# Kernel optimization log

Hardware: AMD Instinct MI355X
Metric: run time of the kernel (lower is better)

## Reference

```python
import jax, jax.numpy as jnp
from jax import lax
import numpy as np

NUM_POINT = 1024
RADIUS = 0.4
NSAMPLE = 32


def setup_inputs() -> dict:
    key = jax.random.key(0)
    ks = jax.random.split(key, 16)
    B, N, C = 8, 16384, 64
    chans = [67, 64, 128, 256]
    inp = {
        "points_xyz": jax.random.normal(ks[0], (B, N, 3), jnp.float32),
        "features": jax.random.normal(ks[1], (B, C, N), jnp.float32),
    }
    ki = 2
    for l, (cin, cout) in enumerate(zip(chans[:-1], chans[1:])):
        inp[f"W{l}"] = jax.random.normal(ks[ki], (cout, cin), jnp.float32) * (1.0 / np.sqrt(cin)); ki += 1
        inp[f"b{l}"] = jax.random.normal(ks[ki], (cout,), jnp.float32) * 0.02; ki += 1
        inp[f"s{l}"] = jax.random.uniform(ks[ki], (cout,), jnp.float32, 0.5, 1.5); ki += 1
        inp[f"t{l}"] = jax.random.normal(ks[ki], (cout,), jnp.float32) * 0.02; ki += 1
    return inp


def farthest_point_sample(xyz, npoint):
    # xyz: (B, N, 3) -> idx (B, npoint) int32. D-FPS starting at index 0.
    B, N, _ = xyz.shape

    def step(carry, _):
        dists, farthest = carry  # (B,N), (B,)
        centroid = jnp.take_along_axis(xyz, farthest[:, None, None], axis=1)  # (B,1,3)
        d = jnp.sum((xyz - centroid) ** 2, axis=-1)  # (B,N)
        dists = jnp.minimum(dists, d)
        nxt = jnp.argmax(dists, axis=-1).astype(jnp.int32)
        return (dists, nxt), farthest

    init = (jnp.full((B, N), 1e10, xyz.dtype), jnp.zeros((B,), jnp.int32))
    _, idx = lax.scan(step, init, None, length=npoint)
    return idx.T  # (B, npoint)


def ball_query(points_xyz, new_xyz, radius, nsample):
    # First-nsample-in-index-order points within radius; pad with first found
    # (semantics of the CUDA ball_query kernel in PointNet++/mmdet3d).
    B, N, _ = points_xyz.shape
    d2 = jnp.sum((new_xyz[:, :, None, :] - points_xyz[:, None, :, :]) ** 2, axis=-1)  # (B,M,N)
    arange = jnp.arange(N, dtype=jnp.float32)
    key = jnp.where(d2 <= radius * radius, arange, jnp.float32(N))
    neg_k, _ = lax.top_k(-key, nsample)  # smallest nsample keys
    idx = (-neg_k).astype(jnp.int32)  # (B,M,K)
    first = idx[..., :1]
    idx = jnp.where(idx < N, idx, first)  # pad empty slots with first neighbor
    return jnp.clip(idx, 0, N - 1)


def query_and_group(points_xyz, new_xyz, features, idx, use_xyz=True):
    # points_xyz (B,N,3), new_xyz (B,M,3), features (B,C,N), idx (B,M,K)
    B, N, _ = points_xyz.shape
    M, K = idx.shape[1], idx.shape[2]
    flat = idx.reshape(B, M * K)
    gxyz = jnp.take_along_axis(points_xyz, flat[:, :, None], axis=1).reshape(B, M, K, 3)
    gxyz = gxyz - new_xyz[:, :, None, :]  # relative coords
    gxyz = jnp.transpose(gxyz, (0, 3, 1, 2))  # (B,3,M,K)
    gfeat = jnp.take_along_axis(features, flat[:, None, :], axis=2).reshape(B, -1, M, K)
    if use_xyz:
        return jnp.concatenate([gxyz, gfeat], axis=1)  # (B, 3+C, M, K)
    return gfeat


def mlp_layer(x, W, b, s, t):
    # 1x1 Conv2d + folded BatchNorm (per-channel scale/shift) + ReLU
    y = jnp.einsum("oc,bcmk->bomk", W, x) + b[None, :, None, None]
    y = y * s[None, :, None, None] + t[None, :, None, None]
    return jax.nn.relu(y)


def reference(points_xyz, features, W0, b0, s0, t0, W1, b1, s1, t1, W2, b2, s2, t2):
    indices = farthest_point_sample(points_xyz, NUM_POINT)  # (B,M)
    new_xyz = jnp.take_along_axis(points_xyz, indices[:, :, None], axis=1)  # (B,M,3)
    idx = ball_query(points_xyz, new_xyz, RADIUS, NSAMPLE)  # (B,M,K)
    g = query_and_group(points_xyz, new_xyz, features, idx, use_xyz=True)  # (B,67,M,K)
    h = mlp_layer(g, W0, b0, s0, t0)
    h = mlp_layer(h, W1, b1, s1, t1)
    h = mlp_layer(h, W2, b2, s2, t2)  # (B,256,M,K)
    new_features = jnp.max(h, axis=-1)  # max pool over K -> (B,256,M)
    return new_xyz, new_features, indices
```

## Files before the change

### kernel.cpp

```cpp
#include <hip/hip_runtime.h>
#include <stdint.h>

#define NB 8
#define NPT 16384
#define NM 1024
#define NK 32

#define WS_W0T 0
#define WS_B0  (WS_W0T + 4288)
#define WS_W1T (WS_B0 + 64)
#define WS_B1  (WS_W1T + 8192)
#define WS_W2T (WS_B1 + 128)
#define WS_B2  (WS_W2T + 32768)
#define WS_IDX (WS_B2 + 256)
#define WS_NXYZ (WS_IDX + 8192)
#define WS_BALL (WS_NXYZ + 24576)

#define OUT_XYZ 0
#define OUT_FEAT 24576
#define OUT_IDX (24576 + 2097152)

__global__ void prep_weights(const float* __restrict__ W0, const float* __restrict__ b0,
                             const float* __restrict__ s0, const float* __restrict__ t0,
                             const float* __restrict__ W1, const float* __restrict__ b1,
                             const float* __restrict__ s1, const float* __restrict__ t1,
                             const float* __restrict__ W2, const float* __restrict__ b2,
                             const float* __restrict__ s2, const float* __restrict__ t2,
                             float* __restrict__ ws) {
    int id = blockIdx.x * 256 + threadIdx.x;
    if (id < 4288) { int c = id >> 6, o = id & 63;  ws[WS_W0T + id] = W0[o * 67 + c] * s0[o]; return; }
    id -= 4288;
    if (id < 64)   { ws[WS_B0 + id] = fmaf(b0[id], s0[id], t0[id]); return; }
    id -= 64;
    if (id < 8192) { int c = id >> 7, o = id & 127; ws[WS_W1T + id] = W1[o * 64 + c] * s1[o]; return; }
    id -= 8192;
    if (id < 128)  { ws[WS_B1 + id] = fmaf(b1[id], s1[id], t1[id]); return; }
    id -= 128;
    if (id < 32768){ int c = id >> 8, o = id & 255; ws[WS_W2T + id] = W2[o * 128 + c] * s2[o]; return; }
    id -= 32768;
    if (id < 256)  { ws[WS_B2 + id] = fmaf(b2[id], s2[id], t2[id]); return; }
}

#define FOREACH16(M) M(0) M(1) M(2) M(3) M(4) M(5) M(6) M(7) \
                     M(8) M(9) M(10) M(11) M(12) M(13) M(14) M(15)

template <int CTRL>
__device__ __forceinline__ uint32_t dpp_max_step(uint32_t v) {
    uint32_t o = (uint32_t)__builtin_amdgcn_update_dpp((int)v, (int)v, CTRL, 0xf, 0xf, false);
    return v > o ? v : o;
}
__device__ __forceinline__ uint32_t wave_max_u32(uint32_t v) {
    v = dpp_max_step<0x111>(v);
    v = dpp_max_step<0x112>(v);
    v = dpp_max_step<0x114>(v);
    v = dpp_max_step<0x118>(v);
    v = dpp_max_step<0x142>(v);
    v = dpp_max_step<0x143>(v);
    return v;
}
__device__ __forceinline__ uint32_t row_max_u32(uint32_t v) {
    v = dpp_max_step<0x111>(v);
    v = dpp_max_step<0x112>(v);
    v = dpp_max_step<0x114>(v);
    v = dpp_max_step<0x118>(v);
    return v;
}

__global__ __attribute__((amdgpu_flat_work_group_size(1024, 1024)))
void fps10_kernel(const float* __restrict__ xyz, int* __restrict__ out_idx) {
    __shared__ float2 pxy[NPT];
    __shared__ uint2 s_red[2][16];
    int b = blockIdx.x, t = threadIdx.x;
    const float* __restrict__ Xp = xyz + (size_t)b * NPT * 3;

#define DECL_PT(j) float pz##j, dd##j;
    FOREACH16(DECL_PT)
#undef DECL_PT

#define LOAD_PT(j) { int p = t + (j) * 1024; \
        float x = Xp[p * 3 + 0], y = Xp[p * 3 + 1]; \
        pz##j = Xp[p * 3 + 2]; \
        pxy[p] = make_float2(x, y); \
        dd##j = 1e10f; }
    FOREACH16(LOAD_PT)
#undef LOAD_PT
    __syncthreads();

    int farthest = 0;
    float cx = Xp[0], cy = Xp[1], cz = Xp[2];
    int lane = t & 63, w = t >> 6;
    for (int it = 0; it < NM; ++it) {
        if (t == 0) out_idx[b * NM + it] = farthest;
        float best = -1.0f; int bi = 0;
#define STEP_PT(j) { \
        float2 q = pxy[t + (j) * 1024]; \
        float dx = __fsub_rn(q.x, cx); \
        float dy = __fsub_rn(q.y, cy); \
        float dz = __fsub_rn(pz##j, cz); \
        float d  = __fadd_rn(__fadd_rn(__fmul_rn(dx, dx), __fmul_rn(dy, dy)), __fmul_rn(dz, dz)); \
        dd##j = fminf(dd##j, d); \
        if (dd##j > best) { best = dd##j; bi = t + (j) * 1024; } }
        FOREACH16(STEP_PT)
#undef STEP_PT
        uint32_t bbits = __float_as_uint(best);
        uint32_t wmax = __builtin_amdgcn_readlane(wave_max_u32(bbits), 63);
        uint32_t cand = (bbits == wmax) ? ~(uint32_t)bi : 0u;
        uint32_t cwin = __builtin_amdgcn_readlane(wave_max_u32(cand), 63);
        if (lane == 0) s_red[it & 1][w] = make_uint2(cwin, wmax);
        __syncthreads();
        uint2 e = s_red[it & 1][lane & 15];
        uint32_t hmax = __builtin_amdgcn_readlane(row_max_u32(e.y), 15);
        uint32_t c2 = (e.y == hmax) ? e.x : 0u;
        uint32_t c2w = __builtin_amdgcn_readlane(row_max_u32(c2), 15);
        int widx = (int)(~c2w);
        farthest = widx;
        float2 cc = pxy[widx];
        cx = cc.x; cy = cc.y;
        cz = Xp[(size_t)widx * 3 + 2];
    }
}

__global__ void gather_newxyz(const float* __restrict__ xyz, const int* __restrict__ idx_ws,
                              float* __restrict__ nxyz_ws, float* __restrict__ out_xyz,
                              float* __restrict__ out_idx_f) {
    int id = blockIdx.x * 256 + threadIdx.x;
    if (id >= NB * NM) return;
    int b = id / NM;
    int p = idx_ws[id];
    const float* Xp = xyz + ((size_t)b * NPT + p) * 3;
    float x = Xp[0], y = Xp[1], z = Xp[2];
    nxyz_ws[id * 3 + 0] = x; nxyz_ws[id * 3 + 1] = y; nxyz_ws[id * 3 + 2] = z;
    out_xyz[id * 3 + 0] = x; out_xyz[id * 3 + 1] = y; out_xyz[id * 3 + 2] = z;
    out_idx_f[id] = (float)p;
}

__global__ __launch_bounds__(256) void ball_query_kernel(const float* __restrict__ xyz,
                                                         const float* __restrict__ nxyz,
                                                         int* __restrict__ ball) {
    int blk = blockIdx.x;
    int b = blk >> 10;
    int t = threadIdx.x;
    const float* Xp = xyz + (size_t)b * NPT * 3;
    float cx = nxyz[blk * 3 + 0], cy = nxyz[blk * 3 + 1], cz = nxyz[blk * 3 + 2];
    const float r2 = (float)(0.4 * 0.4);
    uint64_t mask = 0;
    int base = t * 64;
    const float4* q = (const float4*)(Xp + (size_t)base * 3);
#pragma unroll 4
    for (int c = 0; c < 16; c++) {
        float4 A = q[c * 3 + 0], B = q[c * 3 + 1], C = q[c * 3 + 2];
        float xs[4] = {A.x, A.w, B.z, C.y};
        float ys[4] = {A.y, B.x, B.w, C.z};
        float zs[4] = {A.z, B.y, C.x, C.w};
#pragma unroll
        for (int u = 0; u < 4; u++) {
            float dx = __fsub_rn(xs[u], cx);
            float dy = __fsub_rn(ys[u], cy);
            float dz = __fsub_rn(zs[u], cz);
            float d2 = __fadd_rn(__fadd_rn(__fmul_rn(dx, dx), __fmul_rn(dy, dy)), __fmul_rn(dz, dz));
            if (d2 <= r2) mask |= (1ull << (c * 4 + u));
        }
    }
    int cnt = __popcll(mask);
    int scan = cnt;
    for (int off = 1; off < 64; off <<= 1) {
        int nv = __shfl_up(scan, off);
        if ((t & 63) >= off) scan += nv;
    }
    __shared__ int s_wsum[4];
    __shared__ int s_hit[32];
    int w = t >> 6;
    if ((t & 63) == 63) s_wsum[w] = scan;
    __syncthreads();
    int woff = 0;
    for (int i = 0; i < 4; i++) if (i < w) woff += s_wsum[i];
    int excl = woff + scan - cnt;
    uint64_t mm = mask; int pos = excl;
    while (mm && pos < 32) {
        int j = __ffsll((long long)mm) - 1;
        s_hit[pos] = base + j;
        pos++;
        mm &= mm - 1;
    }
    __syncthreads();
    int total = s_wsum[0] + s_wsum[1] + s_wsum[2] + s_wsum[3];
    if (t < 32) {
        int first = s_hit[0];
        ball[blk * NK + t] = (t < total) ? s_hit[t] : first;
    }
}

__global__ __attribute__((amdgpu_flat_work_group_size(256, 256), amdgpu_waves_per_eu(3, 3)))
void fused_mlp_kernel(const float* __restrict__ xyz,
                      const float* __restrict__ feats,
                      const float* __restrict__ ws_f,
                      const int* __restrict__ ball,
                      const float* __restrict__ nxyz,
                      float* __restrict__ out_feat) {
    int blk = blockIdx.x;
    int b = blk >> 9;
    int m0 = (blk & 511) * 2;
    int t = threadIdx.x;
    int k = t & 31, g = t >> 5;
    __shared__ float u[2][128][32];
    __shared__ float h1[2][64][32];
    __shared__ int sidx[2][32];
    const float* W0t = ws_f + WS_W0T; const float* b0f = ws_f + WS_B0;
    const float* W1t = ws_f + WS_W1T; const float* b1f = ws_f + WS_B1;
    const float* W2t = ws_f + WS_W2T; const float* b2f = ws_f + WS_B2;

    if (t < 64) {
        int ctr = t >> 5;
        sidx[ctr][t & 31] = ball[((size_t)b * NM + m0 + ctr) * NK + (t & 31)];
    }
    __syncthreads();

    const float* Xp = xyz + (size_t)b * NPT * 3;
    if (g < 6) {
        int ctr = g / 3, dim = g % 3;
        float cc = nxyz[((size_t)b * NM + m0 + ctr) * 3 + dim];
        u[ctr][dim][k] = Xp[sidx[ctr][k] * 3 + dim] - cc;
    }
    const float* Fp = feats + (size_t)b * 64 * NPT;
#pragma unroll
    for (int i = 0; i < 8; i++) {
        int c = g + 8 * i;
        u[0][3 + c][k] = Fp[(size_t)c * NPT + sidx[0][k]];
        u[1][3 + c][k] = Fp[(size_t)c * NPT + sidx[1][k]];
    }
    __syncthreads();

    {
        float acc0[8], acc1[8];
#pragma unroll
        for (int i = 0; i < 8; i++) { acc0[i] = b0f[g * 8 + i]; acc1[i] = acc0[i]; }
#pragma unroll 4
        for (int c = 0; c < 67; c++) {
            float xv0 = u[0][c][k], xv1 = u[1][c][k];
            const float* wr = W0t + c * 64 + g * 8;
            float4 wa = *(const float4*)(wr), wb = *(const float4*)(wr + 4);
            acc0[0] = fmaf(wa.x, xv0, acc0[0]); acc1[0] = fmaf(wa.x, xv1, acc1[0]);
            acc0[1] = fmaf(wa.y, xv0, acc0[1]); acc1[1] = fmaf(wa.y, xv1, acc1[1]);
            acc0[2] = fmaf(wa.z, xv0, acc0[2]); acc1[2] = fmaf(wa.z, xv1, acc1[2]);
            acc0[3] = fmaf(wa.w, xv0, acc0[3]); acc1[3] = fmaf(wa.w, xv1, acc1[3]);
            acc0[4] = fmaf(wb.x, xv0, acc0[4]); acc1[4] = fmaf(wb.x, xv1, acc1[4]);
            acc0[5] = fmaf(wb.y, xv0, acc0[5]); acc1[5] = fmaf(wb.y, xv1, acc1[5]);
            acc0[6] = fmaf(wb.z, xv0, acc0[6]); acc1[6] = fmaf(wb.z, xv1, acc1[6]);
            acc0[7] = fmaf(wb.w, xv0, acc0[7]); acc1[7] = fmaf(wb.w, xv1, acc1[7]);
        }
#pragma unroll
        for (int i = 0; i < 8; i++) {
            h1[0][g * 8 + i][k] = fmaxf(acc0[i], 0.0f);
            h1[1][g * 8 + i][k] = fmaxf(acc1[i], 0.0f);
        }
    }
    __syncthreads();

    {
        float acc0[16], acc1[16];
#pragma unroll
        for (int i = 0; i < 16; i++) { acc0[i] = b1f[g * 16 + i]; acc1[i] = acc0[i]; }
#pragma unroll 4
        for (int c = 0; c < 64; c++) {
            float xv0 = h1[0][c][k], xv1 = h1[1][c][k];
            const float4* wr = (const float4*)(W1t + c * 128 + g * 16);
#pragma unroll
            for (int q = 0; q < 4; q++) {
                float4 wv = wr[q];
                acc0[q * 4 + 0] = fmaf(wv.x, xv0, acc0[q * 4 + 0]); acc1[q * 4 + 0] = fmaf(wv.x, xv1, acc1[q * 4 + 0]);
                acc0[q * 4 + 1] = fmaf(wv.y, xv0, acc0[q * 4 + 1]); acc1[q * 4 + 1] = fmaf(wv.y, xv1, acc1[q * 4 + 1]);
                acc0[q * 4 + 2] = fmaf(wv.z, xv0, acc0[q * 4 + 2]); acc1[q * 4 + 2] = fmaf(wv.z, xv1, acc1[q * 4 + 2]);
                acc0[q * 4 + 3] = fmaf(wv.w, xv0, acc0[q * 4 + 3]); acc1[q * 4 + 3] = fmaf(wv.w, xv1, acc1[q * 4 + 3]);
            }
        }
        __syncthreads();
#pragma unroll
        for (int i = 0; i < 16; i++) {
            u[0][g * 16 + i][k] = fmaxf(acc0[i], 0.0f);
            u[1][g * 16 + i][k] = fmaxf(acc1[i], 0.0f);
        }
    }
    __syncthreads();

#pragma unroll
    for (int half = 0; half < 2; half++) {
        float acc0[16], acc1[16];
#pragma unroll
        for (int i = 0; i < 16; i++) { acc0[i] = b2f[g * 32 + half * 16 + i]; acc1[i] = acc0[i]; }
#pragma unroll 4
        for (int c = 0; c < 128; c++) {
            float xv0 = u[0][c][k], xv1 = u[1][c][k];
            const float4* wr = (const float4*)(W2t + c * 256 + g * 32 + half * 16);
#pragma unroll
            for (int q = 0; q < 4; q++) {
                float4 wv = wr[q];
                acc0[q * 4 + 0] = fmaf(wv.x, xv0, acc0[q * 4 + 0]); acc1[q * 4 + 0] = fmaf(wv.x, xv1, acc1[q * 4 + 0]);
                acc0[q * 4 + 1] = fmaf(wv.y, xv0, acc0[q * 4 + 1]); acc1[q * 4 + 1] = fmaf(wv.y, xv1, acc1[q * 4 + 1]);
                acc0[q * 4 + 2] = fmaf(wv.z, xv0, acc0[q * 4 + 2]); acc1[q * 4 + 2] = fmaf(wv.z, xv1, acc1[q * 4 + 2]);
                acc0[q * 4 + 3] = fmaf(wv.w, xv0, acc0[q * 4 + 3]); acc1[q * 4 + 3] = fmaf(wv.w, xv1, acc1[q * 4 + 3]);
            }
        }
#pragma unroll
        for (int i = 0; i < 16; i++) {
            float v0 = fmaxf(acc0[i], 0.0f);
            float v1 = fmaxf(acc1[i], 0.0f);
#pragma unroll
            for (int off = 16; off >= 1; off >>= 1) {
                v0 = fmaxf(v0, __shfl_xor(v0, off));
                v1 = fmaxf(v1, __shfl_xor(v1, off));
            }
            if (k == 0) {
                size_t o = (size_t)b * 256 + g * 32 + half * 16 + i;
                out_feat[o * NM + m0]     = v0;
                out_feat[o * NM + m0 + 1] = v1;
            }
        }
    }
}

extern "C" void kernel_launch(void* const* d_in, const int* in_sizes, int n_in,
                              void* d_out, int out_size, void* d_ws, size_t ws_size,
                              hipStream_t stream) {
    const float* xyz   = (const float*)d_in[0];
    const float* feats = (const float*)d_in[1];
    const float* W0 = (const float*)d_in[2];  const float* b0 = (const float*)d_in[3];
    const float* s0 = (const float*)d_in[4];  const float* t0 = (const float*)d_in[5];
    const float* W1 = (const float*)d_in[6];  const float* b1 = (const float*)d_in[7];
    const float* s1 = (const float*)d_in[8];  const float* t1 = (const float*)d_in[9];
    const float* W2 = (const float*)d_in[10]; const float* b2 = (const float*)d_in[11];
    const float* s2 = (const float*)d_in[12]; const float* t2 = (const float*)d_in[13];

    float* ws_f = (float*)d_ws;
    int*   idx_ws  = (int*)(ws_f + WS_IDX);
    float* nxyz_ws = ws_f + WS_NXYZ;
    int*   ball_ws = (int*)(ws_f + WS_BALL);

    float* out_f = (float*)d_out;
    float* out_xyz  = out_f + OUT_XYZ;
    float* out_feat = out_f + OUT_FEAT;
    float* out_idxf = out_f + OUT_IDX;

    prep_weights<<<179, 256, 0, stream>>>(W0, b0, s0, t0, W1, b1, s1, t1, W2, b2, s2, t2, ws_f);
    fps10_kernel<<<NB, 1024, 0, stream>>>(xyz, idx_ws);
    gather_newxyz<<<32, 256, 0, stream>>>(xyz, idx_ws, nxyz_ws, out_xyz, out_idxf);
    ball_query_kernel<<<NB * NM, 256, 0, stream>>>(xyz, nxyz_ws, ball_ws);
    fused_mlp_kernel<<<NB * NM / 2, 256, 0, stream>>>(xyz, feats, ws_f, ball_ws, nxyz_ws, out_feat);
}
```

Before: 2.690 ms.

## Make MLP weight indices wave-uniform so weights load as scalar operands

Each 64-lane wavefront in the fused MLP kernel now covers both centers (32 samples each) and a group of 16 output channels chosen by wave index. readfirstlane makes the weight offset wave-uniform, so the compiler can fetch weights with scalar loads and broadcast them instead of issuing per-lane vector loads. This also drops the doubled per-center accumulators, which lowers register pressure. The cost is more passes over the input activations per thread in layers 2 and 3.

```diff
diff --git a/kernel.cpp b/kernel.cpp
--- a/kernel.cpp
+++ b/kernel.cpp
@@ -202,6 +202,8 @@
     int m0 = (blk & 511) * 2;
     int t = threadIdx.x;
     int k = t & 31, g = t >> 5;
+    int lane = t & 63, wv = t >> 6;
+    int ctr = lane >> 5, k2 = lane & 31;
     __shared__ float u[2][128][32];
     __shared__ float h1[2][64][32];
     __shared__ int sidx[2][32];
@@ -210,16 +212,16 @@
     const float* W2t = ws_f + WS_W2T; const float* b2f = ws_f + WS_B2;
 
     if (t < 64) {
-        int ctr = t >> 5;
-        sidx[ctr][t & 31] = ball[((size_t)b * NM + m0 + ctr) * NK + (t & 31)];
+        int c2 = t >> 5;
+        sidx[c2][t & 31] = ball[((size_t)b * NM + m0 + c2) * NK + (t & 31)];
     }
     __syncthreads();
 
     const float* Xp = xyz + (size_t)b * NPT * 3;
     if (g < 6) {
-        int ctr = g / 3, dim = g % 3;
-        float cc = nxyz[((size_t)b * NM + m0 + ctr) * 3 + dim];
-        u[ctr][dim][k] = Xp[sidx[ctr][k] * 3 + dim] - cc;
+        int c2 = g / 3, dim = g % 3;
+        float cc = nxyz[((size_t)b * NM + m0 + c2) * 3 + dim];
+        u[c2][dim][k] = Xp[sidx[c2][k] * 3 + dim] - cc;
     }
     const float* Fp = feats + (size_t)b * 64 * NPT;
 #pragma unroll
@@ -231,88 +233,61 @@
     __syncthreads();
 
     {
-        float acc0[8], acc1[8];
-#pragma unroll
-        for (int i = 0; i < 8; i++) { acc0[i] = b0f[g * 8 + i]; acc1[i] = acc0[i]; }
+        int ob = __builtin_amdgcn_readfirstlane(wv * 16);
+        float acc[16];
+#pragma unroll
+        for (int i = 0; i < 16; i++) acc[i] = b0f[ob + i];
 #pragma unroll 4
         for (int c = 0; c < 67; c++) {
-            float xv0 = u[0][c][k], xv1 = u[1][c][k];
-            const float* wr = W0t + c * 64 + g * 8;
-            float4 wa = *(const float4*)(wr), wb = *(const float4*)(wr + 4);
-            acc0[0] = fmaf(wa.x, xv0, acc0[0]); acc1[0] = fmaf(wa.x, xv1, acc1[0]);
-            acc0[1] = fmaf(wa.y, xv0, acc0[1]); acc1[1] = fmaf(wa.y, xv1, acc1[1]);
-            acc0[2] = fmaf(wa.z, xv0, acc0[2]); acc1[2] = fmaf(wa.z, xv1, acc1[2]);
-            acc0[3] = fmaf(wa.w, xv0, acc0[3]); acc1[3] = fmaf(wa.w, xv1, acc1[3]);
-            acc0[4] = fmaf(wb.x, xv0, acc0[4]); acc1[4] = fmaf(wb.x, xv1, acc1[4]);
-            acc0[5] = fmaf(wb.y, xv0, acc0[5]); acc1[5] = fmaf(wb.y, xv1, acc1[5]);
-            acc0[6] = fmaf(wb.z, xv0, acc0[6]); acc1[6] = fmaf(wb.z, xv1, acc1[6]);
-            acc0[7] = fmaf(wb.w, xv0, acc0[7]); acc1[7] = fmaf(wb.w, xv1, acc1[7]);
-        }
-#pragma unroll
-        for (int i = 0; i < 8; i++) {
-            h1[0][g * 8 + i][k] = fmaxf(acc0[i], 0.0f);
-            h1[1][g * 8 + i][k] = fmaxf(acc1[i], 0.0f);
-        }
-    }
-    __syncthreads();
-
-    {
-        float acc0[16], acc1[16];
-#pragma unroll
-        for (int i = 0; i < 16; i++) { acc0[i] = b1f[g * 16 + i]; acc1[i] = acc0[i]; }
+            float xv = u[ctr][c][k2];
+            const float* wr = W0t + c * 64 + ob;
+#pragma unroll
+            for (int i = 0; i < 16; i++) acc[i] = fmaf(wr[i], xv, acc[i]);
+        }
+#pragma unroll
+        for (int i = 0; i < 16; i++) h1[ctr][ob + i][k2] = fmaxf(acc[i], 0.0f);
+    }
+    __syncthreads();
+
+#pragma unroll
+    for (int p = 0; p < 2; p++) {
+        int ob = __builtin_amdgcn_readfirstlane(wv * 16 + p * 64);
+        float acc[16];
+#pragma unroll
+        for (int i = 0; i < 16; i++) acc[i] = b1f[ob + i];
 #pragma unroll 4
         for (int c = 0; c < 64; c++) {
-            float xv0 = h1[0][c][k], xv1 = h1[1][c][k];
-            const float4* wr = (const float4*)(W1t + c * 128 + g * 16);
-#pragma unroll
-            for (int q = 0; q < 4; q++) {
-                float4 wv = wr[q];
-                acc0[q * 4 + 0] = fmaf(wv.x, xv0, acc0[q * 4 + 0]); acc1[q * 4 + 0] = fmaf(wv.x, xv1, acc1[q * 4 + 0]);
-                acc0[q * 4 + 1] = fmaf(wv.y, xv0, acc0[q * 4 + 1]); acc1[q * 4 + 1] = fmaf(wv.y, xv1, acc1[q * 4 + 1]);
-                acc0[q * 4 + 2] = fmaf(wv.z, xv0, acc0[q * 4 + 2]); acc1[q * 4 + 2] = fmaf(wv.z, xv1, acc1[q * 4 + 2]);
-                acc0[q * 4 + 3] = fmaf(wv.w, xv0, acc0[q * 4 + 3]); acc1[q * 4 + 3] = fmaf(wv.w, xv1, acc1[q * 4 + 3]);
-            }
-        }
-        __syncthreads();
-#pragma unroll
-        for (int i = 0; i < 16; i++) {
-            u[0][g * 16 + i][k] = fmaxf(acc0[i], 0.0f);
-            u[1][g * 16 + i][k] = fmaxf(acc1[i], 0.0f);
-        }
-    }
-    __syncthreads();
-
-#pragma unroll
-    for (int half = 0; half < 2; half++) {
-        float acc0[16], acc1[16];
-#pragma unroll
-        for (int i = 0; i < 16; i++) { acc0[i] = b2f[g * 32 + half * 16 + i]; acc1[i] = acc0[i]; }
+            float xv = h1[ctr][c][k2];
+            const float* wr = W1t + c * 128 + ob;
+#pragma unroll
+            for (int i = 0; i < 16; i++) acc[i] = fmaf(wr[i], xv, acc[i]);
+        }
+#pragma unroll
+        for (int i = 0; i < 16; i++) u[ctr][ob + i][k2] = fmaxf(acc[i], 0.0f);
+    }
+    __syncthreads();
+
+#pragma unroll
+    for (int p = 0; p < 4; p++) {
+        int ob = __builtin_amdgcn_readfirstlane(wv * 16 + p * 64);
+        float acc[16];
+#pragma unroll
+        for (int i = 0; i < 16; i++) acc[i] = b2f[ob + i];
 #pragma unroll 4
         for (int c = 0; c < 128; c++) {
-            float xv0 = u[0][c][k], xv1 = u[1][c][k];
-            const float4* wr = (const float4*)(W2t + c * 256 + g * 32 + half * 16);
-#pragma unroll
-            for (int q = 0; q < 4; q++) {
-                float4 wv = wr[q];
-                acc0[q * 4 + 0] = fmaf(wv.x, xv0, acc0[q * 4 + 0]); acc1[q * 4 + 0] = fmaf(wv.x, xv1, acc1[q * 4 + 0]);
-                acc0[q * 4 + 1] = fmaf(wv.y, xv0, acc0[q * 4 + 1]); acc1[q * 4 + 1] = fmaf(wv.y, xv1, acc1[q * 4 + 1]);
-                acc0[q * 4 + 2] = fmaf(wv.z, xv0, acc0[q * 4 + 2]); acc1[q * 4 + 2] = fmaf(wv.z, xv1, acc1[q * 4 + 2]);
-                acc0[q * 4 + 3] = fmaf(wv.w, xv0, acc0[q * 4 + 3]); acc1[q * 4 + 3] = fmaf(wv.w, xv1, acc1[q * 4 + 3]);
-            }
+            float xv = u[ctr][c][k2];
+            const float* wr = W2t + c * 256 + ob;
+#pragma unroll
+            for (int i = 0; i < 16; i++) acc[i] = fmaf(wr[i], xv, acc[i]);
         }
 #pragma unroll
         for (int i = 0; i < 16; i++) {
-            float v0 = fmaxf(acc0[i], 0.0f);
-            float v1 = fmaxf(acc1[i], 0.0f);
-#pragma unroll
-            for (int off = 16; off >= 1; off >>= 1) {
-                v0 = fmaxf(v0, __shfl_xor(v0, off));
-                v1 = fmaxf(v1, __shfl_xor(v1, off));
-            }
-            if (k == 0) {
-                size_t o = (size_t)b * 256 + g * 32 + half * 16 + i;
-                out_feat[o * NM + m0]     = v0;
-                out_feat[o * NM + m0 + 1] = v1;
+            float v = fmaxf(acc[i], 0.0f);
+#pragma unroll
+            for (int off = 16; off >= 1; off >>= 1) v = fmaxf(v, __shfl_xor(v, off));
+            if (k2 == 0) {
+                size_t o = (size_t)b * 256 + ob + i;
+                out_feat[o * NM + m0 + ctr] = v;
             }
         }
     }
```

After: 2.451 ms. 1.1x faster.
